# Optimization experiments

Hardware: AMD Instinct MI355X
Metric: run time of the kernel (lower is better)

The kernel has to match this reference:

```python
import jax, jax.numpy as jnp
import numpy as np

B, C, T, Q = 4, 64, 128, 128   # batch, channels (emb_dim), frames, freq bins
K = 8                          # unfold kernel size (stride 1)
H = 128                        # SRU hidden size per direction
D_IN = C * K                   # SRU input size after unfold
L = Q - K + 1                  # unfolded sequence length
EPS = 1e-5


def setup_inputs() -> dict:
    key = jax.random.key(0)
    ks = jax.random.split(key, 6)
    s = 0.02
    return {
        "features": jax.random.normal(ks[0], (B, C, T, Q), jnp.float32),
        "ln_gamma": jnp.ones((C,), jnp.float32),
        "ln_beta": jnp.zeros((C,), jnp.float32),
        # SRU per-direction weights: W maps D_IN -> [x_tilde | f_gate | r_gate | highway], each H wide
        "w_fwd": jax.random.normal(ks[1], (D_IN, 4 * H), jnp.float32) * s,
        "b_fwd": jnp.zeros((2 * H,), jnp.float32),   # [b_f | b_r]
        "w_bwd": jax.random.normal(ks[2], (D_IN, 4 * H), jnp.float32) * s,
        "b_bwd": jnp.zeros((2 * H,), jnp.float32),
        # ConvTranspose1d weight in PyTorch layout [in_ch=2H, out_ch=C, K]
        "ct_w": jax.random.normal(ks[3], (2 * H, C, K), jnp.float32) * s,
        "ct_b": jnp.zeros((C,), jnp.float32),
    }


def _sru_dir(seq, W, b, reverse):
    """One SRU direction. seq: [N, L, D_IN] -> h: [N, L, H].
    c_t = f_t*c_{t-1} + (1-f_t)*x~_t ;  h_t = r_t*tanh(c_t) + (1-r_t)*x'_t
    (x' is the highway projection since input dim != hidden dim)."""
    U = seq @ W                                   # [N, L, 4H] -- dominant GEMM
    xt, f_pre, r_pre, xp = jnp.split(U, 4, axis=-1)
    bf, br = jnp.split(b, 2)
    f = jax.nn.sigmoid(f_pre + bf)
    r = jax.nn.sigmoid(r_pre + br)
    u = (1.0 - f) * xt
    if reverse:
        f = jnp.flip(f, 1)
        u = jnp.flip(u, 1)
    def combine(x, y):  # linear recurrence c = a*c_prev + b, y is the later element
        return (x[0] * y[0], x[1] * y[0] + y[1])
    c = jax.lax.associative_scan(combine, (f, u), axis=1)[1]
    if reverse:
        c = jnp.flip(c, 1)
    return r * jnp.tanh(c) + (1.0 - r) * xp


def reference(features, ln_gamma, ln_beta, w_fwd, b_fwd, w_bwd, b_bwd, ct_w, ct_b):
    # LayerNorm([C,1,1]): normalize over channel dim per (b,t,q)
    mu = jnp.mean(features, axis=1, keepdims=True)
    var = jnp.var(features, axis=1, keepdims=True)
    x = (features - mu) * jax.lax.rsqrt(var + EPS)
    x = x * ln_gamma[None, :, None, None] + ln_beta[None, :, None, None]

    N = B * T
    x = x.transpose(0, 2, 1, 3).reshape(N, C, Q)          # [B*T, C, Q]
    # nn.Unfold((K,1), stride 1): channel-major patch layout -> [N, C*K, L]
    u = jnp.stack([x[:, :, i:i + L] for i in range(K)], axis=2).reshape(N, C * K, L)
    seq = u.transpose(0, 2, 1)                            # [N, L, C*K]

    h = jnp.concatenate(
        [_sru_dir(seq, w_fwd, b_fwd, False), _sru_dir(seq, w_bwd, b_bwd, True)],
        axis=-1,
    )                                                      # [N, L, 2H]

    # ConvTranspose1d(2H -> C, K, stride=1) == full correlation with flipped kernel
    rhs = jnp.flip(ct_w, -1).transpose(1, 0, 2)           # [C, 2H, K]
    y = jax.lax.conv_general_dilated(
        h.transpose(0, 2, 1), rhs, (1,), [(K - 1, K - 1)],
        dimension_numbers=("NCH", "OIH", "NCH"),
    ) + ct_b[None, :, None]                               # [N, C, Q]

    y = y.reshape(B, T, C, Q).transpose(0, 2, 1, 3)       # [B, C, T, Q]
    return y + features
```

## Files before the change

### kernel.cpp

```cpp
#include <hip/hip_runtime.h>
#include <math.h>

#define BB 4
#define CC 64
#define TT 128
#define QQ 128
#define KK 8
#define HH 128
#define NN 512
#define LL 121
#define LPAD 135

typedef unsigned short ushort;
typedef __attribute__((ext_vector_type(8))) short short8;
typedef __attribute__((ext_vector_type(4))) float f32x4;
typedef __attribute__((ext_vector_type(4))) float float4v;

#define GLP(p) ((const __attribute__((address_space(1))) void*)(p))
#define LDP(p) ((__attribute__((address_space(3))) void*)(p))

__device__ __forceinline__ ushort f2bf(float x) {
  unsigned u = __float_as_uint(x);
  unsigned r = (u + 0x7FFFu + ((u >> 16) & 1u)) >> 16;
  return (ushort)r;
}

__global__ __launch_bounds__(256)
void prep_all(const float* __restrict__ f, const float* __restrict__ gamma,
              const float* __restrict__ beta, const float* __restrict__ wf,
              const float* __restrict__ wb, const float* __restrict__ ctw,
              ushort* __restrict__ xT, ushort* __restrict__ Wt,
              ushort* __restrict__ Bct, ushort* __restrict__ zpage) {
  int bid = blockIdx.x, tid = threadIdx.x;
  if (bid < 256) {
    int p = bid * 256 + tid;
    int q = p & (QQ - 1);
    int t = (p >> 7) & (TT - 1);
    int b = p >> 14;
    const float* base = f + (size_t)b * CC * TT * QQ + (size_t)t * QQ + q;
    float v[64];
#pragma unroll
    for (int c = 0; c < 64; ++c) v[c] = base[(size_t)c * TT * QQ];
    float s = 0.f, s2 = 0.f;
#pragma unroll
    for (int c = 0; c < 64; ++c) { s += v[c]; s2 += v[c] * v[c]; }
    float mu = s * (1.f / CC);
    float var = s2 * (1.f / CC) - mu * mu;
    float rs = rsqrtf(var + 1e-5f);
    int n = b * TT + t;
    ushort* dst = xT + (size_t)n * (CC * QQ) + (size_t)q * CC;
#pragma unroll
    for (int v8 = 0; v8 < 8; ++v8) {
      short8 ov;
#pragma unroll
      for (int e = 0; e < 8; ++e) {
        int c = v8 * 8 + e;
        ov[e] = (short)f2bf((v[c] - mu) * rs * gamma[c] + beta[c]);
      }
      *(short8*)(dst + v8 * 8) = ov;
    }
  } else if (bid < 2816) {
    int idx = (bid - 256) * 256 + tid;
    if (idx < 524288) {
      int r = idx >> 9, d = idx & 511;
      int k = d >> 6, c = d & 63;
      int dir = r >> 9, t = r & 511;
      int h = (t >> 7) * 32 + ((t >> 6) & 1) * 16 + (t & 15);
      int quad = (t >> 4) & 3;
      const float* w = dir ? wb : wf;
      Wt[idx] = f2bf(w[(size_t)(c * 8 + k) * 512 + quad * 128 + h]);
    } else {
      int i2 = idx - 524288;
      int c = i2 >> 11, d = i2 & 2047;
      int k = d >> 8, j = d & 255;
      Bct[i2] = f2bf(ctw[(size_t)j * (CC * KK) + c * KK + k]);
    }
  } else {
    if (tid < 128) ((unsigned*)zpage)[tid] = 0u;
  }
}

__global__ __launch_bounds__(256, 2)
void gemm_mfma(const ushort* __restrict__ xT, const ushort* __restrict__ Wt,
               const float* __restrict__ b_fwd, const float* __restrict__ b_bwd,
               ushort* __restrict__ hp, int n0) {
  __shared__ __align__(16) char smem[51200];
  ushort* Hs = (ushort*)smem;
  ushort* Bs = (ushort*)(smem + 18432);

  int tid = threadIdx.x;
  int nl = blockIdx.y;
  int r0 = blockIdx.x * 256;
  int lane = tid & 63, w = tid >> 6;
  int lrow = lane & 15, lk = lane >> 4;
  f32x4 acc[8][4] = {};
  const ushort* xTn = xT + (size_t)(n0 + nl) * (CC * QQ);

#pragma unroll
  for (int i = 0; i < 4; ++i) {
    int p = i * 256 + tid;
    int row = p >> 3, s3 = p & 7;
    int key = ((row >> 3) ^ row) & 7;
    const ushort* g = xTn + (size_t)row * CC + (s3 ^ key) * 8;
    ushort* l = &Hs[(size_t)(i * 256 + (tid & 192)) * 8];
    __builtin_amdgcn_global_load_lds(GLP(g), LDP(l), 16, 0, 0);
  }
  if (tid < 128) {
    int p = 1024 + tid;
    int row = p >> 3, s3 = p & 7;
    int srow = row < 135 ? row : 134;
    int key = ((row >> 3) ^ row) & 7;
    const ushort* g = xTn + (size_t)srow * CC + (s3 ^ key) * 8;
    ushort* l = &Hs[(size_t)(1024 + (tid & 64)) * 8];
    __builtin_amdgcn_global_load_lds(GLP(g), LDP(l), 16, 0, 0);
  }

#define GEMM_BSTAGE(KS)                                                   \
  {                                                                       \
    _Pragma("unroll")                                                     \
    for (int i = 0; i < 8; ++i) {                                         \
      int p = i * 256 + tid;                                              \
      int row = p >> 3, s3 = (p & 7) ^ (row & 7);                         \
      const ushort* g = Wt + (size_t)(r0 + row) * 512 + (KS) * 64 + s3 * 8; \
      ushort* l = &Bs[(size_t)(i * 256 + (tid & 192)) * 8];               \
      __builtin_amdgcn_global_load_lds(GLP(g), LDP(l), 16, 0, 0);         \
    }                                                                     \
  }

  GEMM_BSTAGE(0);
  __syncthreads();
  int RLb = ((lrow & 0x0C) << 3) | (lrow & 3);
  for (int ks = 0; ks < 8; ++ks) {
#pragma unroll
    for (int s = 0; s < 2; ++s) {
      short8 a[8], b[4];
#pragma unroll
      for (int m = 0; m < 8; ++m) {
        int R = RLb + m * 4 + ks;
        int key = ((R >> 3) ^ R) & 7;
        int slot = (s * 4 + lk) ^ key;
        a[m] = *(const short8*)&Hs[R * 64 + slot * 8];
      }
#pragma unroll
      for (int nn = 0; nn < 4; ++nn) {
        int j = w * 64 + nn * 16 + lrow;
        int slot = (s * 4 + lk) ^ (j & 7);
        b[nn] = *(const short8*)&Bs[j * 64 + slot * 8];
      }
#pragma unroll
      for (int m = 0; m < 8; ++m)
#pragma unroll
        for (int nn = 0; nn < 4; ++nn)
          acc[m][nn] = __builtin_amdgcn_mfma_f32_16x16x32_bf16(
              a[m], b[nn], acc[m][nn], 0, 0, 0);
    }
    if (ks < 7) {
      __syncthreads();
      GEMM_BSTAGE(ks + 1);
      __syncthreads();
    }
  }
#undef GEMM_BSTAGE

  int dirf = r0 >> 9;
  int hgroup = ((r0 & 511) >> 7) + (w >> 1);
  int h = hgroup * 32 + (w & 1) * 16 + lrow;
  const float* bias = dirf ? b_bwd : b_fwd;
  float bf = bias[h], br = bias[128 + h];

  float F = 1.f, U = 0.f;
  if (dirf == 0) {
#pragma unroll
    for (int m = 0; m < 8; ++m)
#pragma unroll
      for (int g = 0; g < 4; ++g) {
        int l = lk * 32 + m * 4 + g;
        float xt = acc[m][0][g], fp = acc[m][1][g];
        float fg = 1.f / (1.f + __expf(-(fp + bf)));
        float u = (1.f - fg) * xt;
        if (l > 120) { fg = 1.f; u = 0.f; }
        U = fg * U + u;
        F = fg * F;
        acc[m][0][g] = F; acc[m][1][g] = U;
      }
  } else {
#pragma unroll
    for (int m = 7; m >= 0; --m)
#pragma unroll
      for (int g = 3; g >= 0; --g) {
        int l = lk * 32 + m * 4 + g;
        float xt = acc[m][0][g], fp = acc[m][1][g];
        float fg = 1.f / (1.f + __expf(-(fp + bf)));
        float u = (1.f - fg) * xt;
        if (l > 120) { fg = 1.f; u = 0.f; }
        U = fg * U + u;
        F = fg * F;
        acc[m][0][g] = F; acc[m][1][g] = U;
      }
  }
  int e = dirf ? 3 - lk : lk;
  float lpU = 0.f;
#pragma unroll
  for (int j = 0; j < 4; ++j) {
    int jl = dirf ? 3 - j : j;
    float tF = __shfl(F, (jl << 4) + lrow);
    float tU = __shfl(U, (jl << 4) + lrow);
    if (j < e) lpU = tF * lpU + tU;
  }
  float cinit = lpU;
  ushort* hpn = hp + (size_t)nl * LPAD * 256;
  int colbase = dirf * 128 + hgroup * 32 + (w & 1) * 16;
#pragma unroll
  for (int m = 0; m < 8; ++m) {
#pragma unroll
    for (int g = 0; g < 4; ++g) {
      int l = lk * 32 + m * 4 + g;
      float c = acc[m][1][g] + acc[m][0][g] * cinit;
      float rp = acc[m][2][g];
      float rg = 1.f / (1.f + __expf(-(rp + br)));
      float e2 = __expf(2.f * c);
      float th = (e2 - 1.f) / (e2 + 1.f);
      float ho = rg * th + (1.f - rg) * acc[m][3][g];
      hpn[(size_t)(l + 7) * 256 + colbase + lrow] = f2bf(ho);
    }
  }
}

__global__ __launch_bounds__(256)
void conv_mfma(const ushort* __restrict__ hp, const ushort* __restrict__ Bct,
               const ushort* __restrict__ zpage, const float* __restrict__ ctb,
               const float* __restrict__ feat, float* __restrict__ out, int n0) {
  __shared__ __align__(16) ushort Hs[144 * 128];
  __shared__ __align__(16) ushort Bs[2][64 * 64];
  int tid = threadIdx.x;
  int nl = blockIdx.x;
  int lane = tid & 63, w = tid >> 6;
  int wr0 = (w >> 1) * 64, wc0 = (w & 1) * 32;
  int lrow = lane & 15, lk = lane >> 4;
  f32x4 acc[4][2] = {};
  const ushort* hpn = hp + (size_t)nl * LPAD * 256;

#define CONV_BSTAGE(T, BSEL)                                               \
  {                                                                        \
    int kk_ = (T) >> 1, sub_ = (T) & 1;                                    \
    _Pragma("unroll")                                                      \
    for (int i = 0; i < 2; ++i) {                                          \
      int p = i * 256 + tid;                                               \
      int row = p >> 3, ds = p & 7;                                        \
      const ushort* g = Bct + (size_t)row * 2048 + kk_ * 256 + jh * 128    \
                      + sub_ * 64 + (ds ^ (row & 7)) * 8;                  \
      ushort* l = &Bs[BSEL][(size_t)(i * 256 + (tid & 192)) * 8];          \
      __builtin_amdgcn_global_load_lds(GLP(g), LDP(l), 16, 0, 0);          \
    }                                                                      \
  }

  for (int jh = 0; jh < 2; ++jh) {
#pragma unroll
    for (int r = 0; r < 9; ++r) {
      int p = r * 256 + tid;
      int row = p >> 4, ds = p & 15;
      int cs = (ds & 8) | ((ds & 7) ^ (row & 7));
      const ushort* g = ((unsigned)(row - 7) <= 120u)
          ? hpn + (size_t)row * 256 + jh * 128 + cs * 8
          : zpage;
      ushort* l = &Hs[(size_t)(r * 256 + (tid & 192)) * 8];
      __builtin_amdgcn_global_load_lds(GLP(g), LDP(l), 16, 0, 0);
    }
    CONV_BSTAGE(0, 0);
    __syncthreads();
    for (int t = 0; t < 16; ++t) {
      int cur = t & 1;
      if (t < 15) CONV_BSTAGE(t + 1, cur ^ 1);
      int kk = t >> 1, sub = t & 1;
#pragma unroll
      for (int s = 0; s < 2; ++s) {
        short8 a[4], b[2];
#pragma unroll
        for (int m = 0; m < 4; ++m) {
          int row = wr0 + m * 16 + lrow + 7 - kk;
          int slot = (sub * 8) | ((s * 4 + lk) ^ (row & 7));
          a[m] = *(const short8*)&Hs[row * 128 + slot * 8];
        }
#pragma unroll
        for (int nn = 0; nn < 2; ++nn) {
          int c = wc0 + nn * 16 + lrow;
          int slot = (s * 4 + lk) ^ (c & 7);
          b[nn] = *(const short8*)&Bs[cur][c * 64 + slot * 8];
        }
#pragma unroll
        for (int m = 0; m < 4; ++m)
#pragma unroll
          for (int nn = 0; nn < 2; ++nn)
            acc[m][nn] = __builtin_amdgcn_mfma_f32_16x16x32_bf16(
                a[m], b[nn], acc[m][nn], 0, 0, 0);
      }
      __syncthreads();
    }
  }
#undef CONV_BSTAGE
  int n = n0 + nl;
  int b = n >> 7, t = n & 127;
#pragma unroll
  for (int m = 0; m < 4; ++m) {
    int q0 = wr0 + m * 16 + lk * 4;
#pragma unroll
    for (int nn = 0; nn < 2; ++nn) {
      int c = wc0 + nn * 16 + lrow;
      size_t idx = (size_t)b * (CC * TT * QQ) + (size_t)c * (TT * QQ)
                 + (size_t)t * QQ + q0;
      float4v fv = *(const float4v*)&feat[idx];
      float cb = ctb[c];
      float4v ov;
#pragma unroll
      for (int g = 0; g < 4; ++g) ov[g] = acc[m][nn][g] + cb + fv[g];
      *(float4v*)&out[idx] = ov;
    }
  }
}

extern "C" void kernel_launch(void* const* d_in, const int* in_sizes, int n_in,
                              void* d_out, int out_size, void* d_ws, size_t ws_size,
                              hipStream_t stream) {
  const float* feat  = (const float*)d_in[0];
  const float* gamma = (const float*)d_in[1];
  const float* beta  = (const float*)d_in[2];
  const float* w_fwd = (const float*)d_in[3];
  const float* b_fwd = (const float*)d_in[4];
  const float* w_bwd = (const float*)d_in[5];
  const float* b_bwd = (const float*)d_in[6];
  const float* ct_w  = (const float*)d_in[7];
  const float* ct_b  = (const float*)d_in[8];
  float* out = (float*)d_out;

  char* wsb = (char*)d_ws;
  ushort* xT  = (ushort*)wsb;
  ushort* Wt  = (ushort*)(wsb + 8389632);
  ushort* Bct = (ushort*)(wsb + 9438208);
  ushort* zpg = (ushort*)(wsb + 9700352);
  size_t persist = 9700864;
  size_t per_n = 69120u;
  int NC = 4;
  for (int cand = 512; cand >= 4; cand >>= 1) {
    if (persist + (size_t)cand * per_n <= ws_size) { NC = cand; break; }
  }
  ushort* hpc = (ushort*)(wsb + persist);

  prep_all<<<dim3(2817), dim3(256), 0, stream>>>(feat, gamma, beta, w_fwd,
                                                 w_bwd, ct_w, xT, Wt, Bct, zpg);

  for (int n0 = 0; n0 < NN; n0 += NC) {
    gemm_mfma<<<dim3(4, NC), dim3(256), 0, stream>>>(xT, Wt, b_fwd, b_bwd,
                                                     hpc, n0);
    conv_mfma<<<dim3(NC), dim3(256), 0, stream>>>(hpc, Bct, zpg, ct_b, feat,
                                                  out, n0);
  }
}
```

Before: 121.7 us.

## Double-buffer weight tiles in LDS with half-size stages to overlap loads

Splits each 64-wide K stage of the weight tile into two 32-wide halves and ping-pongs them between two LDS buffers. The next half-stage is prefetched before the MFMAs on the current one run, which cuts the two barriers per stage down to one and overlaps global-to-LDS loads with compute. It uses a new 4-slot XOR swizzle for the B tile. In exchange there are twice as many loop iterations and barriers overall, and the second buffer needs more LDS.

```diff
diff --git a/kernel.cpp b/kernel.cpp
--- a/kernel.cpp
+++ b/kernel.cpp
@@ -115,50 +115,49 @@
     __builtin_amdgcn_global_load_lds(GLP(g), LDP(l), 16, 0, 0);
   }
 
-#define GEMM_BSTAGE(KS)                                                   \
+#define GEMM_BSTAGE(KS, BSEL)                                             \
   {                                                                       \
+    int tap_ = (KS) >> 1, ch_ = (KS) & 1;                                 \
     _Pragma("unroll")                                                     \
-    for (int i = 0; i < 8; ++i) {                                         \
+    for (int i = 0; i < 4; ++i) {                                         \
       int p = i * 256 + tid;                                              \
-      int row = p >> 3, s3 = (p & 7) ^ (row & 7);                         \
-      const ushort* g = Wt + (size_t)(r0 + row) * 512 + (KS) * 64 + s3 * 8; \
-      ushort* l = &Bs[(size_t)(i * 256 + (tid & 192)) * 8];               \
+      int row = p >> 2, ci = p & 3;                                       \
+      int key = ((row >> 2) ^ row) & 3;                                   \
+      const ushort* g = Wt + (size_t)(r0 + row) * 512 + tap_ * 64         \
+                      + ch_ * 32 + (ci ^ key) * 8;                        \
+      ushort* l = &Bs[(size_t)((BSEL) * 1024 + i * 256 + (tid & 192)) * 8]; \
       __builtin_amdgcn_global_load_lds(GLP(g), LDP(l), 16, 0, 0);         \
     }                                                                     \
   }
 
-  GEMM_BSTAGE(0);
+  GEMM_BSTAGE(0, 0);
   __syncthreads();
   int RLb = ((lrow & 0x0C) << 3) | (lrow & 3);
-  for (int ks = 0; ks < 8; ++ks) {
-#pragma unroll
-    for (int s = 0; s < 2; ++s) {
-      short8 a[8], b[4];
-#pragma unroll
-      for (int m = 0; m < 8; ++m) {
-        int R = RLb + m * 4 + ks;
-        int key = ((R >> 3) ^ R) & 7;
-        int slot = (s * 4 + lk) ^ key;
-        a[m] = *(const short8*)&Hs[R * 64 + slot * 8];
-      }
-#pragma unroll
-      for (int nn = 0; nn < 4; ++nn) {
-        int j = w * 64 + nn * 16 + lrow;
-        int slot = (s * 4 + lk) ^ (j & 7);
-        b[nn] = *(const short8*)&Bs[j * 64 + slot * 8];
-      }
-#pragma unroll
-      for (int m = 0; m < 8; ++m)
-#pragma unroll
-        for (int nn = 0; nn < 4; ++nn)
-          acc[m][nn] = __builtin_amdgcn_mfma_f32_16x16x32_bf16(
-              a[m], b[nn], acc[m][nn], 0, 0, 0);
-    }
-    if (ks < 7) {
-      __syncthreads();
-      GEMM_BSTAGE(ks + 1);
-      __syncthreads();
-    }
+  for (int ks = 0; ks < 16; ++ks) {
+    int cur = ks & 1;
+    if (ks < 15) GEMM_BSTAGE(ks + 1, cur ^ 1);
+    int tap = ks >> 1, ch = ks & 1;
+    short8 a[8], b[4];
+#pragma unroll
+    for (int m = 0; m < 8; ++m) {
+      int R = RLb + m * 4 + tap;
+      int key = ((R >> 3) ^ R) & 7;
+      int slot = (ch * 4 + lk) ^ key;
+      a[m] = *(const short8*)&Hs[R * 64 + slot * 8];
+    }
+#pragma unroll
+    for (int nn = 0; nn < 4; ++nn) {
+      int j = w * 64 + nn * 16 + lrow;
+      int key = ((j >> 2) ^ j) & 3;
+      b[nn] = *(const short8*)&Bs[(size_t)(cur * 1024 + j * 4 + (lk ^ key)) * 8];
+    }
+#pragma unroll
+    for (int m = 0; m < 8; ++m)
+#pragma unroll
+      for (int nn = 0; nn < 4; ++nn)
+        acc[m][nn] = __builtin_amdgcn_mfma_f32_16x16x32_bf16(
+            a[m], b[nn], acc[m][nn], 0, 0, 0);
+    if (ks < 15) __syncthreads();
   }
 #undef GEMM_BSTAGE
 
```

Measured after the change: 126.3 us. 3.8% more time.

## Load MFMA B-operands directly from global in fragment-packed layout, drop LDS staging

Applied to the files above, without the earlier changes.

The prep kernel now writes the SRU weight matrix and the transposed-conv weights in a layout that matches each lane's MFMA B-fragment. Both the GEMM and conv kernels read B operands straight from global memory (L2-resident) as 16-byte vectors, instead of staging them through LDS. This removes the per-k-step __syncthreads pairs and the LDS traffic for B, and shrinks shared memory, which may allow more blocks per CU. The cost is that MFMA issue now depends on global/L2 load latency with no explicit prefetch, and some B data is re-read across waves.

```diff
diff --git a/kernel.cpp b/kernel.cpp
--- a/kernel.cpp
+++ b/kernel.cpp
@@ -29,8 +29,8 @@
 void prep_all(const float* __restrict__ f, const float* __restrict__ gamma,
               const float* __restrict__ beta, const float* __restrict__ wf,
               const float* __restrict__ wb, const float* __restrict__ ctw,
-              ushort* __restrict__ xT, ushort* __restrict__ Wt,
-              ushort* __restrict__ Bct, ushort* __restrict__ zpage) {
+              ushort* __restrict__ xT, ushort* __restrict__ Bg,
+              ushort* __restrict__ Bc2, ushort* __restrict__ zpage) {
   int bid = blockIdx.x, tid = threadIdx.x;
   if (bid < 256) {
     int p = bid * 256 + tid;
@@ -62,18 +62,28 @@
   } else if (bid < 2816) {
     int idx = (bid - 256) * 256 + tid;
     if (idx < 524288) {
-      int r = idx >> 9, d = idx & 511;
-      int k = d >> 6, c = d & 63;
-      int dir = r >> 9, t = r & 511;
+      int jblk = idx >> 13, r1 = idx & 8191;
+      int ks = r1 >> 10, r2 = r1 & 1023;
+      int s = r2 >> 9, r3 = r2 & 511;
+      int lk = r3 >> 7, r4 = r3 & 127;
+      int jr = r4 >> 3, e = r4 & 7;
+      int j = jblk * 16 + jr;
+      int c = s * 32 + lk * 8 + e;
+      int dir = j >> 9, t = j & 511;
       int h = (t >> 7) * 32 + ((t >> 6) & 1) * 16 + (t & 15);
       int quad = (t >> 4) & 3;
       const float* w = dir ? wb : wf;
-      Wt[idx] = f2bf(w[(size_t)(c * 8 + k) * 512 + quad * 128 + h]);
+      Bg[idx] = f2bf(w[(size_t)(c * 8 + ks) * 512 + quad * 128 + h]);
     } else {
       int i2 = idx - 524288;
-      int c = i2 >> 11, d = i2 & 2047;
-      int k = d >> 8, j = d & 255;
-      Bct[i2] = f2bf(ctw[(size_t)j * (CC * KK) + c * KK + k]);
+      int win = i2 >> 12, r1 = i2 & 4095;
+      int s = r1 >> 11, r2 = r1 & 2047;
+      int lk = r2 >> 9, r3 = r2 & 511;
+      int c = r3 >> 3, e = r3 & 7;
+      int jo = (s * 4 + lk) * 8 + e;
+      int kk = win >> 2, jh = (win >> 1) & 1, sub = win & 1;
+      int j2h = jh * 128 + sub * 64 + jo;
+      Bc2[i2] = f2bf(ctw[(size_t)j2h * (CC * KK) + c * KK + kk]);
     }
   } else {
     if (tid < 128) ((unsigned*)zpage)[tid] = 0u;
@@ -81,12 +91,10 @@
 }
 
 __global__ __launch_bounds__(256, 2)
-void gemm_mfma(const ushort* __restrict__ xT, const ushort* __restrict__ Wt,
+void gemm_mfma(const ushort* __restrict__ xT, const ushort* __restrict__ Bg,
                const float* __restrict__ b_fwd, const float* __restrict__ b_bwd,
                ushort* __restrict__ hp, int n0) {
-  __shared__ __align__(16) char smem[51200];
-  ushort* Hs = (ushort*)smem;
-  ushort* Bs = (ushort*)(smem + 18432);
+  __shared__ __align__(16) ushort Hs[144 * 64];
 
   int tid = threadIdx.x;
   int nl = blockIdx.y;
@@ -114,26 +122,19 @@
     ushort* l = &Hs[(size_t)(1024 + (tid & 64)) * 8];
     __builtin_amdgcn_global_load_lds(GLP(g), LDP(l), 16, 0, 0);
   }
-
-#define GEMM_BSTAGE(KS)                                                   \
-  {                                                                       \
-    _Pragma("unroll")                                                     \
-    for (int i = 0; i < 8; ++i) {                                         \
-      int p = i * 256 + tid;                                              \
-      int row = p >> 3, s3 = (p & 7) ^ (row & 7);                         \
-      const ushort* g = Wt + (size_t)(r0 + row) * 512 + (KS) * 64 + s3 * 8; \
-      ushort* l = &Bs[(size_t)(i * 256 + (tid & 192)) * 8];               \
-      __builtin_amdgcn_global_load_lds(GLP(g), LDP(l), 16, 0, 0);         \
-    }                                                                     \
-  }
-
-  GEMM_BSTAGE(0);
   __syncthreads();
+
   int RLb = ((lrow & 0x0C) << 3) | (lrow & 3);
+  const ushort* Bw = Bg + ((size_t)(blockIdx.x * 16 + w * 4) * 8192)
+                   + lk * 128 + lrow * 8;
+#pragma unroll
   for (int ks = 0; ks < 8; ++ks) {
 #pragma unroll
     for (int s = 0; s < 2; ++s) {
       short8 a[8], b[4];
+#pragma unroll
+      for (int nn = 0; nn < 4; ++nn)
+        b[nn] = *(const short8*)&Bw[(size_t)nn * 8192 + ks * 1024 + s * 512];
 #pragma unroll
       for (int m = 0; m < 8; ++m) {
         int R = RLb + m * 4 + ks;
@@ -142,25 +143,13 @@
         a[m] = *(const short8*)&Hs[R * 64 + slot * 8];
       }
 #pragma unroll
-      for (int nn = 0; nn < 4; ++nn) {
-        int j = w * 64 + nn * 16 + lrow;
-        int slot = (s * 4 + lk) ^ (j & 7);
-        b[nn] = *(const short8*)&Bs[j * 64 + slot * 8];
-      }
-#pragma unroll
       for (int m = 0; m < 8; ++m)
 #pragma unroll
         for (int nn = 0; nn < 4; ++nn)
           acc[m][nn] = __builtin_amdgcn_mfma_f32_16x16x32_bf16(
               a[m], b[nn], acc[m][nn], 0, 0, 0);
     }
-    if (ks < 7) {
-      __syncthreads();
-      GEMM_BSTAGE(ks + 1);
-      __syncthreads();
-    }
-  }
-#undef GEMM_BSTAGE
+  }
 
   int dirf = r0 >> 9;
   int hgroup = ((r0 & 511) >> 7) + (w >> 1);
@@ -227,11 +216,10 @@
 }
 
 __global__ __launch_bounds__(256)
-void conv_mfma(const ushort* __restrict__ hp, const ushort* __restrict__ Bct,
+void conv_mfma(const ushort* __restrict__ hp, const ushort* __restrict__ Bc2,
                const ushort* __restrict__ zpage, const float* __restrict__ ctb,
                const float* __restrict__ feat, float* __restrict__ out, int n0) {
   __shared__ __align__(16) ushort Hs[144 * 128];
-  __shared__ __align__(16) ushort Bs[2][64 * 64];
   int tid = threadIdx.x;
   int nl = blockIdx.x;
   int lane = tid & 63, w = tid >> 6;
@@ -239,22 +227,10 @@
   int lrow = lane & 15, lk = lane >> 4;
   f32x4 acc[4][2] = {};
   const ushort* hpn = hp + (size_t)nl * LPAD * 256;
-
-#define CONV_BSTAGE(T, BSEL)                                               \
-  {                                                                        \
-    int kk_ = (T) >> 1, sub_ = (T) & 1;                                    \
-    _Pragma("unroll")                                                      \
-    for (int i = 0; i < 2; ++i) {                                          \
-      int p = i * 256 + tid;                                               \
-      int row = p >> 3, ds = p & 7;                                        \
-      const ushort* g = Bct + (size_t)row * 2048 + kk_ * 256 + jh * 128    \
-                      + sub_ * 64 + (ds ^ (row & 7)) * 8;                  \
-      ushort* l = &Bs[BSEL][(size_t)(i * 256 + (tid & 192)) * 8];          \
-      __builtin_amdgcn_global_load_lds(GLP(g), LDP(l), 16, 0, 0);          \
-    }                                                                      \
-  }
+  const ushort* Bcw = Bc2 + lk * 512 + (wc0 + lrow) * 8;
 
   for (int jh = 0; jh < 2; ++jh) {
+    if (jh) __syncthreads();
 #pragma unroll
     for (int r = 0; r < 9; ++r) {
       int p = r * 256 + tid;
@@ -266,15 +242,17 @@
       ushort* l = &Hs[(size_t)(r * 256 + (tid & 192)) * 8];
       __builtin_amdgcn_global_load_lds(GLP(g), LDP(l), 16, 0, 0);
     }
-    CONV_BSTAGE(0, 0);
     __syncthreads();
+#pragma unroll
     for (int t = 0; t < 16; ++t) {
-      int cur = t & 1;
-      if (t < 15) CONV_BSTAGE(t + 1, cur ^ 1);
       int kk = t >> 1, sub = t & 1;
+      int win = kk * 4 + jh * 2 + sub;
 #pragma unroll
       for (int s = 0; s < 2; ++s) {
         short8 a[4], b[2];
+#pragma unroll
+        for (int nn = 0; nn < 2; ++nn)
+          b[nn] = *(const short8*)&Bcw[(size_t)(win * 8 + s * 4) * 512 + nn * 128];
 #pragma unroll
         for (int m = 0; m < 4; ++m) {
           int row = wr0 + m * 16 + lrow + 7 - kk;
@@ -282,22 +260,14 @@
           a[m] = *(const short8*)&Hs[row * 128 + slot * 8];
         }
 #pragma unroll
-        for (int nn = 0; nn < 2; ++nn) {
-          int c = wc0 + nn * 16 + lrow;
-          int slot = (s * 4 + lk) ^ (c & 7);
-          b[nn] = *(const short8*)&Bs[cur][c * 64 + slot * 8];
-        }
-#pragma unroll
         for (int m = 0; m < 4; ++m)
 #pragma unroll
           for (int nn = 0; nn < 2; ++nn)
             acc[m][nn] = __builtin_amdgcn_mfma_f32_16x16x32_bf16(
                 a[m], b[nn], acc[m][nn], 0, 0, 0);
       }
-      __syncthreads();
-    }
-  }
-#undef CONV_BSTAGE
+    }
+  }
   int n = n0 + nl;
   int b = n >> 7, t = n & 127;
 #pragma unroll
@@ -334,8 +304,8 @@
 
   char* wsb = (char*)d_ws;
   ushort* xT  = (ushort*)wsb;
-  ushort* Wt  = (ushort*)(wsb + 8389632);
-  ushort* Bct = (ushort*)(wsb + 9438208);
+  ushort* Bg  = (ushort*)(wsb + 8389632);
+  ushort* Bc2 = (ushort*)(wsb + 9438208);
   ushort* zpg = (ushort*)(wsb + 9700352);
   size_t persist = 9700864;
   size_t per_n = 69120u;
@@ -346,12 +316,12 @@
   ushort* hpc = (ushort*)(wsb + persist);
 
   prep_all<<<dim3(2817), dim3(256), 0, stream>>>(feat, gamma, beta, w_fwd,
-                                                 w_bwd, ct_w, xT, Wt, Bct, zpg);
+                                                 w_bwd, ct_w, xT, Bg, Bc2, zpg);
 
   for (int n0 = 0; n0 < NN; n0 += NC) {
-    gemm_mfma<<<dim3(4, NC), dim3(256), 0, stream>>>(xT, Wt, b_fwd, b_bwd,
+    gemm_mfma<<<dim3(4, NC), dim3(256), 0, stream>>>(xT, Bg, b_fwd, b_bwd,
                                                      hpc, n0);
-    conv_mfma<<<dim3(NC), dim3(256), 0, stream>>>(hpc, Bct, zpg, ct_b, feat,
+    conv_mfma<<<dim3(NC), dim3(256), 0, stream>>>(hpc, Bc2, zpg, ct_b, feat,
                                                   out, n0);
   }
 }
```

Result: slower. 222.4 us (+82.7%).
